# Kernel tuning notes

Hardware: AMD Instinct MI355X
Metric: run time of the kernel (lower is better)

The kernel has to match this reference:

```python
import jax, jax.numpy as jnp
import numpy as np

EPSILON = 0.001
CAP = 2000.0
H, W, C, B = 224, 224, 1024, 256


def setup_inputs() -> dict:
    key = jax.random.key(0)
    k1, k2, k3, k4 = jax.random.split(key, 4)
    x = jax.random.normal(k1, (B, H, W), dtype=jnp.float32)
    positions = 0.5 + 0.3 * jax.random.normal(k2, (1, 1, C, 2), dtype=jnp.float32)
    sigmas = 0.02 * jax.random.normal(k3, (1, 1, C), dtype=jnp.float32)
    curve_weights = 0.2 * jax.random.normal(k4, (1, 1, C), dtype=jnp.float32)
    y_axis = jnp.linspace(0.0, 1.0, H + 1)[:-1]
    x_axis = jnp.linspace(0.0, 1.0, W + 1)[:-1]
    ys, xs = jnp.meshgrid(y_axis, x_axis, indexing='ij')
    return {"x": x, "positions": positions, "sigmas": sigmas,
            "curve_weights": curve_weights, "xs": xs.astype(jnp.float32),
            "ys": ys.astype(jnp.float32)}


def calc_curves(positions, sigmas, curve_weights, xs, ys):
    # sigmas/curve_weights: (1,1,C); xs/ys: (H,W)
    two_sig2 = 2.0 * sigmas ** 2 + EPSILON            # (1,1,C)
    factor = 1.0 / (2.0 * jnp.pi * sigmas ** 2 + EPSILON)
    grid = (xs[:, :, None] - positions[..., 1]) ** 2 + \
           (ys[:, :, None] - positions[..., 0]) ** 2   # (H,W,C)
    curves = factor * jnp.exp(-grid / two_sig2) * curve_weights
    return jnp.clip(curves, -CAP, CAP)                 # (H,W,C)


def reference(x, positions, sigmas, curve_weights, xs, ys):
    x = x.reshape(-1, H, W)
    curves = calc_curves(positions, sigmas, curve_weights, xs, ys)
    num_pixels = float(H * W)
    # sum over H,W of curves[None] * x[...,None]  ==  GEMM contraction
    out = jnp.einsum('bhw,hwc->bc', x, curves) / num_pixels
    return out
```

## Files before the change

kernel.cpp:

```cpp
#include <hip/hip_runtime.h>
#include <hip/hip_bf16.h>
#include <stdint.h>

#define HH 224
#define WW 224
#define CC 1024
#define BB 256
#define KK (HH*WW)
#define EPSILON_F 0.001f
#define LOG2E 1.4426950408889634f
#define INVN (1.0f/50176.0f)
#define CLAMP_V (2000.0f/50176.0f)

#define KCHUNKS 32
#define ROWS_PER_CHUNK 7
#define STEPS 49

#define LDS_STRIDE 36

typedef __bf16 bf16x8 __attribute__((ext_vector_type(8)));
typedef float  f32x4  __attribute__((ext_vector_type(4)));

__global__ __launch_bounds__(256)
void cvt_bf16_kernel(const float* __restrict__ x, __hip_bfloat16* __restrict__ xb, int n8) {
    int i = blockIdx.x * 256 + threadIdx.x;
    if (i >= n8) return;
    const float4* p = (const float4*)(x + (size_t)i * 8);
    float4 a = p[0], b = p[1];
    union { __hip_bfloat16 h[8]; uint4 u; } o;
    o.h[0] = (__hip_bfloat16)a.x; o.h[1] = (__hip_bfloat16)a.y;
    o.h[2] = (__hip_bfloat16)a.z; o.h[3] = (__hip_bfloat16)a.w;
    o.h[4] = (__hip_bfloat16)b.x; o.h[5] = (__hip_bfloat16)b.y;
    o.h[6] = (__hip_bfloat16)b.z; o.h[7] = (__hip_bfloat16)b.w;
    *(uint4*)(xb + (size_t)i * 8) = o.u;
}

__global__ __launch_bounds__(256)
void reduce_kernel(const float* __restrict__ part, float* __restrict__ out) {
    int i = blockIdx.x * 256 + threadIdx.x;
    const f32x4* p = (const f32x4*)part + i;
    f32x4 s = {0.f, 0.f, 0.f, 0.f};
#pragma unroll
    for (int z = 0; z < KCHUNKS; ++z)
        s += p[(size_t)z * (BB * CC / 4)];
    ((f32x4*)out)[i] = s;
}

template <bool BF16A, bool PARTIAL>
__global__ __launch_bounds__(256)
void blob_gemm_kernel(const void* __restrict__ xin,
                      const float* __restrict__ pos,
                      const float* __restrict__ sig,
                      const float* __restrict__ cwt,
                      const float* __restrict__ xs,
                      const float* __restrict__ ys,
                      float* __restrict__ dst) {
    __shared__ __bf16 As[2][256 * LDS_STRIDE];
    __shared__ __bf16 Bs[2][64 * LDS_STRIDE];
    __shared__ float  xrow[WW];
    __shared__ float  ycol[ROWS_PER_CHUNK];

    const int tid  = threadIdx.x;
    const int wave = tid >> 6;
    const int lane = tid & 63;

    const int c0 = blockIdx.x * 64;
    const int z  = blockIdx.y;
    const int k0 = z * (ROWS_PER_CHUNK * WW);

    if (tid < WW) xrow[tid] = xs[tid];
    if (tid >= WW && tid < WW + ROWS_PER_CHUNK)
        ycol[tid - WW] = ys[(z * ROWS_PER_CHUNK + (tid - WW)) * WW];

    const int q   = tid & 3;
    const int cr0 = tid >> 2;
    const int c   = c0 + cr0;
    float A2, S2, P0, P1;
    {
        float s  = sig[c];
        float w  = cwt[c];
        float s2 = s * s;
        A2 = w / (6.283185307179586f * s2 + EPSILON_F) * INVN;
        S2 = LOG2E / (2.0f * s2 + EPSILON_F);
        P0 = pos[2 * c];
        P1 = pos[2 * c + 1];
    }

    const __hip_bfloat16* agb[4];
    const float* agf[4];
#pragma unroll
    for (int j = 0; j < 4; ++j) {
        size_t off = (size_t)(cr0 + 64 * j) * KK + k0 + q * 8;
        agb[j] = (const __hip_bfloat16*)xin + off;
        agf[j] = (const float*)xin + off;
    }
    const int as_w = cr0 * LDS_STRIDE + q * 8;
    const int bs_w = cr0 * LDS_STRIDE + q * 8;

    const int wm = wave * 64;
    const int fl = lane & 15;
    const int fk = (lane >> 4) * 8;
    const int ar_off = (wm + fl) * LDS_STRIDE + fk;
    const int br_off = fl * LDS_STRIDE + fk;

    f32x4 acc[4][4];
#pragma unroll
    for (int i = 0; i < 4; ++i)
#pragma unroll
        for (int j = 0; j < 4; ++j) acc[i][j] = (f32x4){0.f, 0.f, 0.f, 0.f};

    __syncthreads();

    float ycolr[ROWS_PER_CHUNK];
#pragma unroll
    for (int r = 0; r < ROWS_PER_CHUNK; ++r) ycolr[r] = ycol[r];

    float Ex[8];
    {
        float4 xv0 = *(const float4*)(xrow + q * 8);
        float4 xv1 = *(const float4*)(xrow + q * 8 + 4);
        float xv[8] = {xv0.x, xv0.y, xv0.z, xv0.w, xv1.x, xv1.y, xv1.z, xv1.w};
#pragma unroll
        for (int i = 0; i < 8; ++i) {
            float dx = xv[i] - P1;
            Ex[i] = __builtin_amdgcn_exp2f(-(dx * S2 * dx));
        }
        float dy  = ycolr[0] - P0;
        float eyA = __builtin_amdgcn_exp2f(-(dy * S2 * dy)) * A2;
        union { __bf16 h[8]; uint4 u; } cv;
#pragma unroll
        for (int i = 0; i < 8; ++i) {
            float v = Ex[i] * eyA;
            cv.h[i] = (__bf16)fminf(fmaxf(v, -CLAMP_V), CLAMP_V);
        }
        *(uint4*)(&Bs[0][bs_w]) = cv.u;
#pragma unroll
        for (int j = 0; j < 4; ++j) {
            union { __bf16 h[8]; uint4 u; } av;
            if (BF16A) {
                av.u = *(const uint4*)(agb[j]);
            } else {
                float4 f0 = *(const float4*)(agf[j]);
                float4 f1 = *(const float4*)(agf[j] + 4);
                av.h[0] = (__bf16)f0.x; av.h[1] = (__bf16)f0.y;
                av.h[2] = (__bf16)f0.z; av.h[3] = (__bf16)f0.w;
                av.h[4] = (__bf16)f1.x; av.h[5] = (__bf16)f1.y;
                av.h[6] = (__bf16)f1.z; av.h[7] = (__bf16)f1.w;
            }
            *(uint4*)(&As[0][as_w + 64 * j * LDS_STRIDE]) = av.u;
        }
    }
    __syncthreads();

    int nr = 1, nwb = 0;
#pragma unroll 2
    for (int s = 0; s < STEPS; ++s) {
        const int cb = s & 1;

        uint4  pa[4];
        float4 pf0[4], pf1[4];
        if (s < STEPS - 1) {
            const int koff = nr * WW + nwb * 32;
            if (BF16A) {
#pragma unroll
                for (int j = 0; j < 4; ++j) pa[j] = *(const uint4*)(agb[j] + koff);
            } else {
#pragma unroll
                for (int j = 0; j < 4; ++j) {
                    pf0[j] = *(const float4*)(agf[j] + koff);
                    pf1[j] = *(const float4*)(agf[j] + koff + 4);
                }
            }
        }

        bf16x8 fa[4], fb[4];
#pragma unroll
        for (int i = 0; i < 4; ++i) {
            fa[i] = *(const bf16x8*)(&As[cb][ar_off + i * 16 * LDS_STRIDE]);
            fb[i] = *(const bf16x8*)(&Bs[cb][br_off + i * 16 * LDS_STRIDE]);
        }
#pragma unroll
        for (int mi = 0; mi < 4; ++mi)
#pragma unroll
            for (int ni = 0; ni < 4; ++ni)
                acc[mi][ni] = __builtin_amdgcn_mfma_f32_16x16x32_bf16(
                    fa[mi], fb[ni], acc[mi][ni], 0, 0, 0);

        if (s < STEPS - 1) {
            if (nr == 0) {
                float4 xv0 = *(const float4*)(xrow + nwb * 32 + q * 8);
                float4 xv1 = *(const float4*)(xrow + nwb * 32 + q * 8 + 4);
                float xv[8] = {xv0.x, xv0.y, xv0.z, xv0.w, xv1.x, xv1.y, xv1.z, xv1.w};
#pragma unroll
                for (int i = 0; i < 8; ++i) {
                    float dx = xv[i] - P1;
                    Ex[i] = __builtin_amdgcn_exp2f(-(dx * S2 * dx));
                }
            }
            float dy  = ycolr[nr] - P0;
            float eyA = __builtin_amdgcn_exp2f(-(dy * S2 * dy)) * A2;
            union { __bf16 h[8]; uint4 u; } cv;
#pragma unroll
            for (int i = 0; i < 8; ++i) {
                float v = Ex[i] * eyA;
                cv.h[i] = (__bf16)fminf(fmaxf(v, -CLAMP_V), CLAMP_V);
            }
            *(uint4*)(&Bs[cb ^ 1][bs_w]) = cv.u;
#pragma unroll
            for (int j = 0; j < 4; ++j) {
                union { __bf16 h[8]; uint4 u; } av;
                if (BF16A) {
                    av.u = pa[j];
                } else {
                    av.h[0] = (__bf16)pf0[j].x; av.h[1] = (__bf16)pf0[j].y;
                    av.h[2] = (__bf16)pf0[j].z; av.h[3] = (__bf16)pf0[j].w;
                    av.h[4] = (__bf16)pf1[j].x; av.h[5] = (__bf16)pf1[j].y;
                    av.h[6] = (__bf16)pf1[j].z; av.h[7] = (__bf16)pf1[j].w;
                }
                *(uint4*)(&As[cb ^ 1][as_w + 64 * j * LDS_STRIDE]) = av.u;
            }
            ++nr;
            if (nr == ROWS_PER_CHUNK) { nr = 0; ++nwb; }
        }
        __syncthreads();
    }

    const int orow = (lane >> 4) * 4;
    float* base = PARTIAL ? (dst + (size_t)z * BB * CC) : dst;
#pragma unroll
    for (int mi = 0; mi < 4; ++mi) {
        int m = wm + mi * 16 + orow;
#pragma unroll
        for (int ni = 0; ni < 4; ++ni) {
            int cc = c0 + ni * 16 + fl;
#pragma unroll
            for (int v = 0; v < 4; ++v) {
                if (PARTIAL)
                    base[(size_t)(m + v) * CC + cc] = acc[mi][ni][v];
                else
                    atomicAdd(base + (size_t)(m + v) * CC + cc, acc[mi][ni][v]);
            }
        }
    }
}

extern "C" void kernel_launch(void* const* d_in, const int* in_sizes, int n_in,
                              void* d_out, int out_size, void* d_ws, size_t ws_size,
                              hipStream_t stream) {
    const float* x   = (const float*)d_in[0];
    const float* pos = (const float*)d_in[1];
    const float* sg  = (const float*)d_in[2];
    const float* cw  = (const float*)d_in[3];
    const float* xs  = (const float*)d_in[4];
    const float* ys  = (const float*)d_in[5];
    float* out = (float*)d_out;

    dim3 grid(CC / 64, KCHUNKS);
    const size_t nx   = (size_t)BB * KK;
    const size_t XB   = nx * sizeof(__hip_bfloat16);
    const size_t PART = (size_t)KCHUNKS * BB * CC * 4;
    const int n8 = (int)(nx / 8);

    if (ws_size >= XB + PART) {
        __hip_bfloat16* xb = (__hip_bfloat16*)d_ws;
        float* part = (float*)((char*)d_ws + XB);
        cvt_bf16_kernel<<<(n8 + 255) / 256, 256, 0, stream>>>(x, xb, n8);
        blob_gemm_kernel<true, true><<<grid, 256, 0, stream>>>(xb, pos, sg, cw, xs, ys, part);
        reduce_kernel<<<BB * CC / 4 / 256, 256, 0, stream>>>(part, out);
    } else if (ws_size >= PART) {
        float* part = (float*)d_ws;
        blob_gemm_kernel<false, true><<<grid, 256, 0, stream>>>(x, pos, sg, cw, xs, ys, part);
        reduce_kernel<<<BB * CC / 4 / 256, 256, 0, stream>>>(part, out);
    } else if (ws_size >= XB) {
        __hip_bfloat16* xb = (__hip_bfloat16*)d_ws;
        hipMemsetAsync(out, 0, (size_t)BB * CC * sizeof(float), stream);
        cvt_bf16_kernel<<<(n8 + 255) / 256, 256, 0, stream>>>(x, xb, n8);
        blob_gemm_kernel<true, false><<<grid, 256, 0, stream>>>(xb, pos, sg, cw, xs, ys, out);
    } else {
        hipMemsetAsync(out, 0, (size_t)BB * CC * sizeof(float), stream);
        blob_gemm_kernel<false, false><<<grid, 256, 0, stream>>>(x, pos, sg, cw, xs, ys, out);
    }
}
```

Before: 158.3 us.

## Load A fragments directly from global, drop partial-sum reduce, XCD-aware split-K grid

Removes the LDS staging of the x (A) operand. Each wave now loads its MFMA A fragments straight from global memory into registers, prefetching one step ahead. The separate partial-buffer reduce kernel is replaced by atomicAdd into a zeroed output. Split-K grows from 32 to 56 chunks, and blocks are mapped so chunks sharing an XCD share the same K range for L2 reuse. This cuts LDS traffic, barriers and the partials write/read, but adds many more fp32 atomics and uncoalesced fragment-shaped global loads.

```diff
diff --git a/kernel.cpp b/kernel.cpp
--- a/kernel.cpp
+++ b/kernel.cpp
@@ -12,9 +12,9 @@
 #define INVN (1.0f/50176.0f)
 #define CLAMP_V (2000.0f/50176.0f)
 
-#define KCHUNKS 32
-#define ROWS_PER_CHUNK 7
-#define STEPS 49
+#define KCHUNKS 56
+#define ROWS_PER_CHUNK 4
+#define STEPS 28
 
 #define LDS_STRIDE 36
 
@@ -35,18 +35,7 @@
     *(uint4*)(xb + (size_t)i * 8) = o.u;
 }
 
-__global__ __launch_bounds__(256)
-void reduce_kernel(const float* __restrict__ part, float* __restrict__ out) {
-    int i = blockIdx.x * 256 + threadIdx.x;
-    const f32x4* p = (const f32x4*)part + i;
-    f32x4 s = {0.f, 0.f, 0.f, 0.f};
-#pragma unroll
-    for (int z = 0; z < KCHUNKS; ++z)
-        s += p[(size_t)z * (BB * CC / 4)];
-    ((f32x4*)out)[i] = s;
-}
-
-template <bool BF16A, bool PARTIAL>
+template <bool BF16A>
 __global__ __launch_bounds__(256)
 void blob_gemm_kernel(const void* __restrict__ xin,
                       const float* __restrict__ pos,
@@ -54,8 +43,7 @@
                       const float* __restrict__ cwt,
                       const float* __restrict__ xs,
                       const float* __restrict__ ys,
-                      float* __restrict__ dst) {
-    __shared__ __bf16 As[2][256 * LDS_STRIDE];
+                      float* __restrict__ out) {
     __shared__ __bf16 Bs[2][64 * LDS_STRIDE];
     __shared__ float  xrow[WW];
     __shared__ float  ycol[ROWS_PER_CHUNK];
@@ -64,9 +52,13 @@
     const int wave = tid >> 6;
     const int lane = tid & 63;
 
-    const int c0 = blockIdx.x * 64;
-    const int z  = blockIdx.y;
-    const int k0 = z * (ROWS_PER_CHUNK * WW);
+    const int id   = blockIdx.x;
+    const int xcd  = id & 7;
+    const int slot = id >> 3;
+    const int z    = xcd * (KCHUNKS / 8) + slot % (KCHUNKS / 8);
+    const int cx   = slot / (KCHUNKS / 8);
+    const int c0   = cx * 64;
+    const int k0   = z * (ROWS_PER_CHUNK * WW);
 
     if (tid < WW) xrow[tid] = xs[tid];
     if (tid >= WW && tid < WW + ROWS_PER_CHUNK)
@@ -85,23 +77,30 @@
         P0 = pos[2 * c];
         P1 = pos[2 * c + 1];
     }
-
-    const __hip_bfloat16* agb[4];
-    const float* agf[4];
-#pragma unroll
-    for (int j = 0; j < 4; ++j) {
-        size_t off = (size_t)(cr0 + 64 * j) * KK + k0 + q * 8;
-        agb[j] = (const __hip_bfloat16*)xin + off;
-        agf[j] = (const float*)xin + off;
-    }
-    const int as_w = cr0 * LDS_STRIDE + q * 8;
     const int bs_w = cr0 * LDS_STRIDE + q * 8;
 
-    const int wm = wave * 64;
     const int fl = lane & 15;
     const int fk = (lane >> 4) * 8;
-    const int ar_off = (wm + fl) * LDS_STRIDE + fk;
+    const int wm = wave * 64;
+    const __hip_bfloat16* afb = (const __hip_bfloat16*)xin + (size_t)(wm + fl) * KK + k0 + fk;
+    const float*          aff = (const float*)xin          + (size_t)(wm + fl) * KK + k0 + fk;
     const int br_off = fl * LDS_STRIDE + fk;
+
+    auto load_afrag = [&](int mi, int koff) -> bf16x8 {
+        if (BF16A) {
+            return *(const bf16x8*)(afb + (size_t)mi * 16 * KK + koff);
+        } else {
+            const float* p = aff + (size_t)mi * 16 * KK + koff;
+            float4 f0 = *(const float4*)(p);
+            float4 f1 = *(const float4*)(p + 4);
+            union { __bf16 h[8]; bf16x8 v; } t;
+            t.h[0] = (__bf16)f0.x; t.h[1] = (__bf16)f0.y;
+            t.h[2] = (__bf16)f0.z; t.h[3] = (__bf16)f0.w;
+            t.h[4] = (__bf16)f1.x; t.h[5] = (__bf16)f1.y;
+            t.h[6] = (__bf16)f1.z; t.h[7] = (__bf16)f1.w;
+            return t.v;
+        }
+    };
 
     f32x4 acc[4][4];
 #pragma unroll
@@ -134,22 +133,10 @@
             cv.h[i] = (__bf16)fminf(fmaxf(v, -CLAMP_V), CLAMP_V);
         }
         *(uint4*)(&Bs[0][bs_w]) = cv.u;
-#pragma unroll
-        for (int j = 0; j < 4; ++j) {
-            union { __bf16 h[8]; uint4 u; } av;
-            if (BF16A) {
-                av.u = *(const uint4*)(agb[j]);
-            } else {
-                float4 f0 = *(const float4*)(agf[j]);
-                float4 f1 = *(const float4*)(agf[j] + 4);
-                av.h[0] = (__bf16)f0.x; av.h[1] = (__bf16)f0.y;
-                av.h[2] = (__bf16)f0.z; av.h[3] = (__bf16)f0.w;
-                av.h[4] = (__bf16)f1.x; av.h[5] = (__bf16)f1.y;
-                av.h[6] = (__bf16)f1.z; av.h[7] = (__bf16)f1.w;
-            }
-            *(uint4*)(&As[0][as_w + 64 * j * LDS_STRIDE]) = av.u;
-        }
-    }
+    }
+    bf16x8 fa[4];
+#pragma unroll
+    for (int mi = 0; mi < 4; ++mi) fa[mi] = load_afrag(mi, 0);
     __syncthreads();
 
     int nr = 1, nwb = 0;
@@ -157,28 +144,17 @@
     for (int s = 0; s < STEPS; ++s) {
         const int cb = s & 1;
 
-        uint4  pa[4];
-        float4 pf0[4], pf1[4];
+        bf16x8 pa[4];
         if (s < STEPS - 1) {
             const int koff = nr * WW + nwb * 32;
-            if (BF16A) {
-#pragma unroll
-                for (int j = 0; j < 4; ++j) pa[j] = *(const uint4*)(agb[j] + koff);
-            } else {
-#pragma unroll
-                for (int j = 0; j < 4; ++j) {
-                    pf0[j] = *(const float4*)(agf[j] + koff);
-                    pf1[j] = *(const float4*)(agf[j] + koff + 4);
-                }
-            }
-        }
-
-        bf16x8 fa[4], fb[4];
-#pragma unroll
-        for (int i = 0; i < 4; ++i) {
-            fa[i] = *(const bf16x8*)(&As[cb][ar_off + i * 16 * LDS_STRIDE]);
-            fb[i] = *(const bf16x8*)(&Bs[cb][br_off + i * 16 * LDS_STRIDE]);
-        }
+#pragma unroll
+            for (int mi = 0; mi < 4; ++mi) pa[mi] = load_afrag(mi, koff);
+        }
+
+        bf16x8 fb[4];
+#pragma unroll
+        for (int ni = 0; ni < 4; ++ni)
+            fb[ni] = *(const bf16x8*)(&Bs[cb][br_off + ni * 16 * LDS_STRIDE]);
 #pragma unroll
         for (int mi = 0; mi < 4; ++mi)
 #pragma unroll
@@ -206,27 +182,17 @@
                 cv.h[i] = (__bf16)fminf(fmaxf(v, -CLAMP_V), CLAMP_V);
             }
             *(uint4*)(&Bs[cb ^ 1][bs_w]) = cv.u;
-#pragma unroll
-            for (int j = 0; j < 4; ++j) {
-                union { __bf16 h[8]; uint4 u; } av;
-                if (BF16A) {
-                    av.u = pa[j];
-                } else {
-                    av.h[0] = (__bf16)pf0[j].x; av.h[1] = (__bf16)pf0[j].y;
-                    av.h[2] = (__bf16)pf0[j].z; av.h[3] = (__bf16)pf0[j].w;
-                    av.h[4] = (__bf16)pf1[j].x; av.h[5] = (__bf16)pf1[j].y;
-                    av.h[6] = (__bf16)pf1[j].z; av.h[7] = (__bf16)pf1[j].w;
-                }
-                *(uint4*)(&As[cb ^ 1][as_w + 64 * j * LDS_STRIDE]) = av.u;
-            }
             ++nr;
             if (nr == ROWS_PER_CHUNK) { nr = 0; ++nwb; }
         }
         __syncthreads();
+        if (s < STEPS - 1) {
+#pragma unroll
+            for (int mi = 0; mi < 4; ++mi) fa[mi] = pa[mi];
+        }
     }
 
     const int orow = (lane >> 4) * 4;
-    float* base = PARTIAL ? (dst + (size_t)z * BB * CC) : dst;
 #pragma unroll
     for (int mi = 0; mi < 4; ++mi) {
         int m = wm + mi * 16 + orow;
@@ -234,12 +200,8 @@
         for (int ni = 0; ni < 4; ++ni) {
             int cc = c0 + ni * 16 + fl;
 #pragma unroll
-            for (int v = 0; v < 4; ++v) {
-                if (PARTIAL)
-                    base[(size_t)(m + v) * CC + cc] = acc[mi][ni][v];
-                else
-                    atomicAdd(base + (size_t)(m + v) * CC + cc, acc[mi][ni][v]);
-            }
+            for (int v = 0; v < 4; ++v)
+                atomicAdd(out + (size_t)(m + v) * CC + cc, acc[mi][ni][v]);
         }
     }
 }
@@ -255,29 +217,18 @@
     const float* ys  = (const float*)d_in[5];
     float* out = (float*)d_out;
 
-    dim3 grid(CC / 64, KCHUNKS);
-    const size_t nx   = (size_t)BB * KK;
-    const size_t XB   = nx * sizeof(__hip_bfloat16);
-    const size_t PART = (size_t)KCHUNKS * BB * CC * 4;
-    const int n8 = (int)(nx / 8);
-
-    if (ws_size >= XB + PART) {
+    hipMemsetAsync(out, 0, (size_t)BB * CC * sizeof(float), stream);
+
+    const int nblk = 16 * KCHUNKS;
+    const size_t nx = (size_t)BB * KK;
+    const size_t XB = nx * sizeof(__hip_bfloat16);
+
+    if (ws_size >= XB) {
         __hip_bfloat16* xb = (__hip_bfloat16*)d_ws;
-        float* part = (float*)((char*)d_ws + XB);
+        int n8 = (int)(nx / 8);
         cvt_bf16_kernel<<<(n8 + 255) / 256, 256, 0, stream>>>(x, xb, n8);
-        blob_gemm_kernel<true, true><<<grid, 256, 0, stream>>>(xb, pos, sg, cw, xs, ys, part);
-        reduce_kernel<<<BB * CC / 4 / 256, 256, 0, stream>>>(part, out);
-    } else if (ws_size >= PART) {
-        float* part = (float*)d_ws;
-        blob_gemm_kernel<false, true><<<grid, 256, 0, stream>>>(x, pos, sg, cw, xs, ys, part);
-        reduce_kernel<<<BB * CC / 4 / 256, 256, 0, stream>>>(part, out);
-    } else if (ws_size >= XB) {
-        __hip_bfloat16* xb = (__hip_bfloat16*)d_ws;
-        hipMemsetAsync(out, 0, (size_t)BB * CC * sizeof(float), stream);
-        cvt_bf16_kernel<<<(n8 + 255) / 256, 256, 0, stream>>>(x, xb, n8);
-        blob_gemm_kernel<true, false><<<grid, 256, 0, stream>>>(xb, pos, sg, cw, xs, ys, out);
+        blob_gemm_kernel<true><<<nblk, 256, 0, stream>>>(xb, pos, sg, cw, xs, ys, out);
     } else {
-        hipMemsetAsync(out, 0, (size_t)BB * CC * sizeof(float), stream);
-        blob_gemm_kernel<false, false><<<grid, 256, 0, stream>>>(x, pos, sg, cw, xs, ys, out);
+        blob_gemm_kernel<false><<<nblk, 256, 0, stream>>>(x, pos, sg, cw, xs, ys, out);
     }
 }
```

Measured after the change: 186.3 us. 1.18x slower.
